# Kernel tuning notes

Hardware: AMD Instinct MI355X
Metric: run time of the kernel (lower is better)

## Reference

```python
import jax, jax.numpy as jnp
import numpy as np

N, E, B, F_IN, C, K = 200000, 3200000, 128, 128, 10, 30
D_CAT = 97  # 32+32+32+1 concatenated GCN outputs


def setup_inputs() -> dict:
    key = jax.random.key(0)
    ks = jax.random.split(key, 12)
    s = 0.1
    return {
        "x": jax.random.normal(ks[0], (N, F_IN), jnp.float32),
        "edge_index": jax.random.randint(ks[1], (2, E), 0, N, jnp.int32),
        "batch": jnp.sort(jax.random.randint(ks[2], (N,), 0, B, jnp.int32)),
        "W1": jax.random.normal(ks[3], (F_IN, 32), jnp.float32) * s,
        "b1": jnp.zeros((32,), jnp.float32),
        "W2": jax.random.normal(ks[4], (32, 32), jnp.float32) * s,
        "b2": jnp.zeros((32,), jnp.float32),
        "W3": jax.random.normal(ks[5], (32, 32), jnp.float32) * s,
        "b3": jnp.zeros((32,), jnp.float32),
        "W4": jax.random.normal(ks[6], (32, 1), jnp.float32) * s,
        "b4": jnp.zeros((1,), jnp.float32),
        "conv5_w": jax.random.normal(ks[7], (16, 1, 97), jnp.float32) * s,
        "conv5_b": jnp.zeros((16,), jnp.float32),
        "conv6_w": jax.random.normal(ks[8], (32, 16, 5), jnp.float32) * s,
        "conv6_b": jnp.zeros((32,), jnp.float32),
        "fc1_w": jax.random.normal(ks[9], (352, 128), jnp.float32) * s,
        "fc1_b": jnp.zeros((128,), jnp.float32),
        "fc2_w": jax.random.normal(ks[10], (128, C), jnp.float32) * s,
        "fc2_b": jnp.zeros((C,), jnp.float32),
    }


def _gcn(x, W, b, src, dst, enorm, self_norm):
    # PyG GCNConv: h = xW; out = sum_j norm_ij * h_j (incl. self loop) + b
    h = x @ W
    agg = jax.ops.segment_sum(h[src] * enorm[:, None], dst, num_segments=h.shape[0])
    return agg + h * self_norm[:, None] + b


def _conv1d(x, w, b, stride):
    y = jax.lax.conv_general_dilated(x, w, (stride,), 'VALID',
                                     dimension_numbers=('NCH', 'OIH', 'NCH'))
    return y + b[None, :, None]


def reference(x, edge_index, batch, W1, b1, W2, b2, W3, b3, W4, b4,
              conv5_w, conv5_b, conv6_w, conv6_b, fc1_w, fc1_b, fc2_w, fc2_b):
    src, dst = edge_index[0], edge_index[1]
    # remove_self_loops (zero edge weight) then GCN adds self loop of weight 1
    w = (src != dst).astype(x.dtype)
    deg = jax.ops.segment_sum(w, dst, num_segments=N) + 1.0
    dinv = jax.lax.rsqrt(deg)
    enorm = w * dinv[src] * dinv[dst]   # per-edge sym norm
    self_norm = 1.0 / deg               # self-loop norm = dinv[i]^2

    x1 = jnp.tanh(_gcn(x, W1, b1, src, dst, enorm, self_norm))
    x2 = jnp.tanh(_gcn(x1, W2, b2, src, dst, enorm, self_norm))
    x3 = jnp.tanh(_gcn(x2, W3, b3, src, dst, enorm, self_norm))
    x4 = jnp.tanh(_gcn(x3, W4, b4, src, dst, enorm, self_norm))
    xc = jnp.concatenate([x1, x2, x3, x4], axis=-1)  # [N, 97]

    # SortAggregation(k=30): per-graph top-k nodes by last channel (descending)
    keyf = xc[:, -1]
    graph_ids = jnp.arange(B, dtype=batch.dtype)
    scores = jnp.where(batch[None, :] == graph_ids[:, None], keyf[None, :],
                       jnp.float32(-jnp.inf))         # [B, N]
    topv, topi = jax.lax.top_k(scores, K)              # [B, K]
    feats = xc[topi]                                   # [B, K, 97]
    feats = jnp.where(jnp.isfinite(topv)[..., None], feats, 0.0)  # pad rows -> 0
    z = feats.reshape(B, 1, K * D_CAT)                 # [B, 1, 2910]

    z = jax.nn.relu(_conv1d(z, conv5_w, conv5_b, 97))  # [B, 16, 30]
    z = jax.lax.reduce_window(z, -jnp.inf, jax.lax.max,
                              (1, 1, 2), (1, 1, 2), 'VALID')  # [B, 16, 15]
    z = jax.nn.relu(_conv1d(z, conv6_w, conv6_b, 1))   # [B, 32, 11]
    z = z.reshape(B, -1)                               # [B, 352]
    h = jax.nn.relu(z @ fc1_w + fc1_b)                 # dropout = identity (eval)
    return jax.nn.log_softmax(h @ fc2_w + fc2_b, axis=-1)
```

## Files before the change

kernel.cpp:

```cpp
#include <hip/hip_runtime.h>
#include <math.h>

#define TPB 256
#define TOPK 30
#define NGRAPH 128
#define TKCAP 4096
#define BSHIFT 11
#define NBMAX 128
#define FSHIFT 8
#define NFMAX 800
#define FCAP 4608


__global__ void bhist(const int* __restrict__ src, const int* __restrict__ dst,
                      int* __restrict__ btot, int E) {
    __shared__ int bcnt[NBMAX];
    int t = threadIdx.x;
    int base = blockIdx.x * 2048;
    int lim = E - base; if (lim > 2048) lim = 2048;
    for (int i = t; i < NBMAX; i += 256) bcnt[i] = 0;
    __syncthreads();
    for (int i = t; i < lim; i += 256) {
        int s = src[base + i], d = dst[base + i];
        if (s != d) atomicAdd(&bcnt[d >> BSHIFT], 1);
    }
    __syncthreads();
    for (int i = t; i < NBMAX; i += 256)
        if (bcnt[i] > 0) atomicAdd(&btot[i], bcnt[i]);
}

__global__ void bucket_scan(const int* __restrict__ btot, int* __restrict__ bbase,
                            int nbuckets) {
    __shared__ int ls[NBMAX];
    int t = threadIdx.x;
    int v = (t < nbuckets) ? btot[t] : 0;
    ls[t] = v;
    __syncthreads();
    for (int o = 1; o < NBMAX; o <<= 1) {
        int x = 0;
        if (t >= o) x = ls[t - o];
        __syncthreads();
        ls[t] += x;
        __syncthreads();
    }
    if (t < nbuckets) bbase[t] = ls[t] - v;
}

__global__ void bin_edges(const int* __restrict__ src, const int* __restrict__ dst,
                          const int* __restrict__ bbase_g, int* __restrict__ gcur,
                          int2* __restrict__ scratch, int E) {
    __shared__ int2 eds[2048];
    __shared__ int bcnt[NBMAX], bbase[NBMAX], boff[NBMAX];
    int t = threadIdx.x;
    int base = blockIdx.x * 2048;
    int lim = E - base; if (lim > 2048) lim = 2048;
    for (int i = t; i < NBMAX; i += 256) { bcnt[i] = 0; boff[i] = 0; }
    __syncthreads();
    for (int i = t; i < lim; i += 256) {
        int s = src[base + i], d = dst[base + i];
        if (s == d) d = -1;
        eds[i] = make_int2(s, d);
        if (d >= 0) atomicAdd(&bcnt[d >> BSHIFT], 1);
    }
    __syncthreads();
    for (int i = t; i < NBMAX; i += 256) {
        if (bcnt[i] > 0)
            bbase[i] = bbase_g[i] + atomicAdd(&gcur[i], bcnt[i]);
    }
    __syncthreads();
    for (int i = t; i < lim; i += 256) {
        int2 ed = eds[i];
        if (ed.y >= 0) {
            int b = ed.y >> BSHIFT;
            int pos = bbase[b] + atomicAdd(&boff[b], 1);
            scratch[pos] = ed;
        }
    }
}

__global__ void bucket_count(const int2* __restrict__ scratch,
                             const int* __restrict__ bbase, const int* __restrict__ btot,
                             int* __restrict__ rowptr, float* __restrict__ dinv,
                             float* __restrict__ snorm, int N, int NB) {
    __shared__ int hist[1 << BSHIFT];
    __shared__ int ls2[256];
    int b = blockIdx.x, t = threadIdx.x;
    int nlo = b << BSHIFT;
    int nn = N - nlo; if (nn > (1 << BSHIFT)) nn = 1 << BSHIFT;
    for (int i = t; i < (1 << BSHIFT); i += 256) hist[i] = 0;
    __syncthreads();
    int lo = bbase[b], hi = lo + btot[b];
    for (int e = lo + t; e < hi; e += 256)
        atomicAdd(&hist[scratch[e].y - nlo], 1);
    __syncthreads();
    int loc[8]; int run = 0;
    #pragma unroll
    for (int j = 0; j < 8; ++j) { loc[j] = run; run += hist[t * 8 + j]; }
    ls2[t] = run;
    __syncthreads();
    for (int o = 1; o < 256; o <<= 1) {
        int x = (t >= o) ? ls2[t - o] : 0;
        __syncthreads();
        ls2[t] += x;
        __syncthreads();
    }
    int base = bbase[b] + ls2[t] - run;
    #pragma unroll
    for (int j = 0; j < 8; ++j) {
        int i = t * 8 + j;
        if (i < nn) {
            rowptr[nlo + i] = base + loc[j];
            int c = hist[i];
            float deg = (float)c + 1.0f;
            dinv[nlo + i] = 1.0f / sqrtf(deg);
            snorm[nlo + i] = 1.0f / deg;
        }
    }
    if (b == NB - 1 && t == 0) rowptr[N] = bbase[b] + btot[b];
}

__global__ void bin2(const int2* __restrict__ scratch, const int* __restrict__ rowptr,
                     int* __restrict__ fcur, int2* __restrict__ scratch2, int N, int E) {
    __shared__ int fcnt[NFMAX], fbase[NFMAX], foff[NFMAX];
    int t = threadIdx.x;
    int En = rowptr[N];
    int base = blockIdx.x * 8192;
    if (base >= En) return;
    int lim = En - base; if (lim > 8192) lim = 8192;
    for (int i = t; i < NFMAX; i += 256) { fcnt[i] = 0; foff[i] = 0; }
    __syncthreads();
    for (int i = t; i < lim; i += 256) {
        int d = scratch[base + i].y;
        atomicAdd(&fcnt[d >> FSHIFT], 1);
    }
    __syncthreads();
    for (int fi = t; fi < NFMAX; fi += 256) {
        if (fcnt[fi] > 0)
            fbase[fi] = rowptr[fi << FSHIFT] + atomicAdd(&fcur[fi], fcnt[fi]);
    }
    __syncthreads();
    for (int i = t; i < lim; i += 256) {
        int2 ed = scratch[base + i];
        int fi = ed.y >> FSHIFT;
        int pos = fbase[fi] + atomicAdd(&foff[fi], 1);
        scratch2[pos] = ed;
    }
}

__global__ __launch_bounds__(256) void scatter_sort(const int2* __restrict__ scratch2,
                                                    const int* __restrict__ rowptr,
                                                    const float* __restrict__ dinv,
                                                    int2* __restrict__ eprec, int N) {
    __shared__ int srcA[FCAP], dstA[FCAP], inv[FCAP];
    __shared__ int hist[1 << FSHIFT];
    __shared__ int hcur[1 << FSHIFT];
    int f = blockIdx.x, t = threadIdx.x;
    int nlo = f << FSHIFT;
    int nhi = nlo + (1 << FSHIFT); if (nhi > N) nhi = N;
    int lo = rowptr[nlo], hi = rowptr[nhi];
    int span = hi - lo;
    for (int i = t; i < (1 << FSHIFT); i += 256) hist[i] = 0;
    __syncthreads();
    if (span <= FCAP) {
        for (int i = t; i < span; i += 256) {
            int2 ed = scratch2[lo + i];
            srcA[i] = ed.x; dstA[i] = ed.y;
            atomicAdd(&hist[ed.y - nlo], 1);
        }
        __syncthreads();
        int v = hist[t];
        hcur[t] = v;
        __syncthreads();
        for (int o = 1; o < 256; o <<= 1) {
            int x = (t >= o) ? hcur[t - o] : 0;
            __syncthreads();
            hcur[t] += x;
            __syncthreads();
        }
        int excl = hcur[t] - v;
        __syncthreads();
        hcur[t] = excl;
        __syncthreads();
        for (int i = t; i < span; i += 256) {
            int slot = atomicAdd(&hcur[dstA[i] - nlo], 1);
            inv[slot] = i;
        }
        __syncthreads();
        for (int p = t; p < span; p += 256) {
            int i = inv[p];
            int s = srcA[i], d = dstA[i];
            eprec[lo + p] = make_int2(s, __float_as_int(dinv[s] * dinv[d]));
        }
    } else {
        for (int e = lo + t; e < hi; e += 256) {
            int2 ed = scratch2[e];
            int d = ed.y;
            int p = rowptr[d] + atomicAdd(&hist[d - nlo], 1);
            eprec[p] = make_int2(ed.x, __float_as_int(dinv[ed.x] * dinv[d]));
        }
    }
}


__global__ void mm_128_32(const float* __restrict__ X, const float* __restrict__ W,
                          float* __restrict__ H, int n) {
    __shared__ float Ws[128 * 32];
    __shared__ float xs[32 * 128];
    int t = threadIdx.x;
    int rbase = blockIdx.x * 32;
    #pragma unroll
    for (int j = 0; j < 4; ++j) {
        int idx = t + 256 * j;
        *(float4*)(Ws + idx * 4) = *(const float4*)(W + idx * 4);
        int row = rbase + (idx >> 5);
        float4 v = make_float4(0.f, 0.f, 0.f, 0.f);
        if (row < n) v = *(const float4*)(X + (long)rbase * 128 + idx * 4);
        *(float4*)(xs + idx * 4) = v;
    }
    __syncthreads();
    int c4 = (t & 7) * 4, r = t >> 3;
    int row = rbase + r;
    if (row >= n) return;
    float ac0 = 0.f, ac1 = 0.f, ac2 = 0.f, ac3 = 0.f;
    #pragma unroll 8
    for (int k0 = 0; k0 < 128; k0 += 4) {
        float4 xv = *(const float4*)(xs + r * 128 + k0);
        #pragma unroll
        for (int j = 0; j < 4; ++j) {
            float xj = (j == 0) ? xv.x : (j == 1) ? xv.y : (j == 2) ? xv.z : xv.w;
            float4 wv = *(const float4*)(Ws + (k0 + j) * 32 + c4);
            ac0 += xj * wv.x; ac1 += xj * wv.y; ac2 += xj * wv.z; ac3 += xj * wv.w;
        }
    }
    *(float4*)(H + (long)row * 32 + c4) = make_float4(ac0, ac1, ac2, ac3);
}

__global__ void mm_32_32(const float* __restrict__ X, const float* __restrict__ W,
                         float* __restrict__ H, int n) {
    __shared__ float Ws[32 * 32];
    __shared__ float xs[32 * 32];
    int t = threadIdx.x;
    int rbase = blockIdx.x * 32;
    {
        *(float4*)(Ws + t * 4) = *(const float4*)(W + t * 4);
        int row = rbase + (t >> 3);
        float4 v = make_float4(0.f, 0.f, 0.f, 0.f);
        if (row < n) v = *(const float4*)(X + (long)rbase * 32 + t * 4);
        *(float4*)(xs + t * 4) = v;
    }
    __syncthreads();
    int c4 = (t & 7) * 4, r = t >> 3;
    int row = rbase + r;
    if (row >= n) return;
    float ac0 = 0.f, ac1 = 0.f, ac2 = 0.f, ac3 = 0.f;
    #pragma unroll
    for (int k0 = 0; k0 < 32; k0 += 4) {
        float4 xv = *(const float4*)(xs + r * 32 + k0);
        #pragma unroll
        for (int j = 0; j < 4; ++j) {
            float xj = (j == 0) ? xv.x : (j == 1) ? xv.y : (j == 2) ? xv.z : xv.w;
            float4 wv = *(const float4*)(Ws + (k0 + j) * 32 + c4);
            ac0 += xj * wv.x; ac1 += xj * wv.y; ac2 += xj * wv.z; ac3 += xj * wv.w;
        }
    }
    *(float4*)(H + (long)row * 32 + c4) = make_float4(ac0, ac1, ac2, ac3);
}

__global__ void mm_32_1(const float* __restrict__ X, const float* __restrict__ W,
                        float* __restrict__ H4, int n) {
    int gid = blockIdx.x * blockDim.x + threadIdx.x;
    int node = gid >> 3, l = gid & 7;
    if (node >= n) return;
    float4 v = *(const float4*)(X + (long)node * 32 + l * 4);
    float s = v.x * W[l * 4] + v.y * W[l * 4 + 1] + v.z * W[l * 4 + 2] + v.w * W[l * 4 + 3];
    s += __shfl_xor(s, 1, 64);
    s += __shfl_xor(s, 2, 64);
    s += __shfl_xor(s, 4, 64);
    if (l == 0) H4[node] = s;
}


__global__ void agg32(const float* __restrict__ H, const int2* __restrict__ eprec,
                      const int* __restrict__ rowptr,
                      const float* __restrict__ snorm, const float* __restrict__ bias,
                      float* __restrict__ OUT, int n) {
    int gid = blockIdx.x * blockDim.x + threadIdx.x;
    int node = gid >> 3, l = gid & 7;
    if (node >= n) return;
    int beg = rowptr[node], end = rowptr[node + 1];
    float ax = 0.f, ay = 0.f, az = 0.f, aw = 0.f;
    int e0 = beg;
    for (; e0 + 8 <= end; e0 += 8) {
        int2 ed = eprec[e0 + l];
        int ss[8]; float ww[8];
        #pragma unroll
        for (int j = 0; j < 8; ++j) {
            ss[j] = __shfl(ed.x, j, 8);
            ww[j] = __shfl(__int_as_float(ed.y), j, 8);
        }
        float4 hv[8];
        #pragma unroll
        for (int j = 0; j < 8; ++j)
            hv[j] = *(const float4*)(H + (long)ss[j] * 32 + l * 4);
        #pragma unroll
        for (int j = 0; j < 8; ++j) {
            ax += hv[j].x * ww[j]; ay += hv[j].y * ww[j];
            az += hv[j].z * ww[j]; aw += hv[j].w * ww[j];
        }
    }
    if (e0 < end) {
        int m = end - e0;
        int2 ed = (l < m) ? eprec[e0 + l] : make_int2(0, 0);
        for (int j = 0; j < m; ++j) {
            int s = __shfl(ed.x, j, 8);
            float w = __shfl(__int_as_float(ed.y), j, 8);
            float4 hv = *(const float4*)(H + (long)s * 32 + l * 4);
            ax += hv.x * w; ay += hv.y * w; az += hv.z * w; aw += hv.w * w;
        }
    }
    float sn = snorm[node];
    float4 hv = *(const float4*)(H + (long)node * 32 + l * 4);
    float4 bv = *(const float4*)(bias + l * 4);
    float4 o;
    o.x = tanhf(ax + hv.x * sn + bv.x);
    o.y = tanhf(ay + hv.y * sn + bv.y);
    o.z = tanhf(az + hv.z * sn + bv.z);
    o.w = tanhf(aw + hv.w * sn + bv.w);
    *(float4*)(OUT + (long)node * 32 + l * 4) = o;
}

__global__ void agg1(const float* __restrict__ H4, const int2* __restrict__ eprec,
                     const int* __restrict__ rowptr,
                     const float* __restrict__ snorm, const float* __restrict__ b4,
                     float* __restrict__ X4, int n) {
    int node = blockIdx.x * blockDim.x + threadIdx.x;
    if (node >= n) return;
    int beg = rowptr[node], end = rowptr[node + 1];
    float acc = 0.f;
    for (int e = beg; e < end; ++e) {
        int2 ed = eprec[e];
        acc += H4[ed.x] * __int_as_float(ed.y);
    }
    X4[node] = tanhf(acc + H4[node] * snorm[node] + b4[0]);
}


__global__ __launch_bounds__(256) void topk_head(
        const float* __restrict__ x1, const float* __restrict__ x2,
        const float* __restrict__ x3, const float* __restrict__ x4,
        const int* __restrict__ batch, int Nn,
        const float* __restrict__ w5, const float* __restrict__ b5,
        const float* __restrict__ w6, const float* __restrict__ b6,
        const float* __restrict__ fw1, const float* __restrict__ fb1,
        const float* __restrict__ fw2, const float* __restrict__ fb2,
        float* __restrict__ out) {
    int g = blockIdx.x;
    int t = threadIdx.x;
    __shared__ int topi_l[TOPK];
    __shared__ int selg[TOPK];
    __shared__ int begend[2];
    __shared__ float vals[TKCAP];
    __shared__ float wbv[4];
    __shared__ int wbi[4];
    __shared__ float feats[TOPK][97];
    __shared__ float c5[16][30];
    __shared__ float p6[16][15];
    __shared__ float z[352];
    __shared__ float hh[128];
    __shared__ float oo[10];

    if (t == 0) {
        int lo = 0, hi = Nn;
        while (lo < hi) { int m = (lo + hi) >> 1; if (batch[m] < g) lo = m + 1; else hi = m; }
        begend[0] = lo;
        lo = 0; hi = Nn;
        while (lo < hi) { int m = (lo + hi) >> 1; if (batch[m] < g + 1) lo = m + 1; else hi = m; }
        begend[1] = lo;
    }
    __syncthreads();
    int beg = begend[0], end = begend[1];
    int range = end - beg;

    if (range <= 2048) {
        if (t < 64) {
            float rv[32];
            #pragma unroll
            for (int j = 0; j < 32; ++j) {
                int i = t + (j << 6);
                rv[j] = (i < range) ? x4[beg + i] : -INFINITY;
            }
            for (int k = 0; k < TOPK; ++k) {
                float best = -INFINITY;
                int bj = -1;
                #pragma unroll
                for (int j = 0; j < 32; ++j)
                    if (rv[j] > best) { best = rv[j]; bj = j; }
                int bi = (bj < 0) ? 0x7fffffff : (bj << 6) + t;
                #pragma unroll
                for (int off = 1; off < 64; off <<= 1) {
                    float ov = __shfl_xor(best, off, 64);
                    int oi = __shfl_xor(bi, off, 64);
                    if (ov > best || (ov == best && oi < bi)) { best = ov; bi = oi; }
                }
                if (t == 0)
                    topi_l[k] = (bi == 0x7fffffff) ? -1 : beg + bi;
                if (bi != 0x7fffffff && (bi & 63) == t) {
                    int wj = bi >> 6;
                    #pragma unroll
                    for (int j = 0; j < 32; ++j)
                        if (j == wj) rv[j] = -INFINITY;
                }
            }
        }
    } else {
        int lim = range < TKCAP ? range : TKCAP;
        for (int i = t; i < lim; i += 256) vals[i] = x4[beg + i];
        __syncthreads();
        for (int k = 0; k < TOPK; ++k) {
            float best = -INFINITY;
            int bi = 0x7fffffff;
            for (int i = t; i < lim; i += 256) {
                float v = vals[i];
                if (v > best) { best = v; bi = i; }
            }
            for (int i = TKCAP + t; i < range; i += 256) {
                int gi = beg + i;
                bool taken = false;
                for (int j = 0; j < k; ++j)
                    if (selg[j] == gi) { taken = true; break; }
                if (taken) continue;
                float v = x4[gi];
                if (v > best || (v == best && i < bi)) { best = v; bi = i; }
            }
            #pragma unroll
            for (int off = 1; off < 64; off <<= 1) {
                float ov = __shfl_xor(best, off, 64);
                int oi = __shfl_xor(bi, off, 64);
                if (ov > best || (ov == best && oi < bi)) { best = ov; bi = oi; }
            }
            if ((t & 63) == 0) { wbv[t >> 6] = best; wbi[t >> 6] = bi; }
            __syncthreads();
            if (t == 0) {
                float bv = wbv[0]; int bi0 = wbi[0];
                for (int wv = 1; wv < 4; ++wv)
                    if (wbv[wv] > bv || (wbv[wv] == bv && wbi[wv] < bi0)) { bv = wbv[wv]; bi0 = wbi[wv]; }
                int gl = (bi0 == 0x7fffffff) ? -1 : beg + bi0;
                selg[k] = gl;
                topi_l[k] = gl;
                if (bi0 != 0x7fffffff && bi0 < TKCAP) vals[bi0] = -INFINITY;
            }
            __syncthreads();
        }
    }
    __syncthreads();

    for (int idx = t; idx < TOPK * 97; idx += 256) {
        int k = idx / 97, j = idx % 97;
        int node = topi_l[k];
        float v = 0.f;
        if (node >= 0) {
            if (j < 32) v = x1[(long)node * 32 + j];
            else if (j < 64) v = x2[(long)node * 32 + (j - 32)];
            else if (j < 96) v = x3[(long)node * 32 + (j - 64)];
            else v = x4[node];
        }
        feats[k][j] = v;
    }
    __syncthreads();

    for (int idx = t; idx < 16 * 30; idx += 256) {
        int oc = idx / 30, k = idx % 30;
        float acc = b5[oc];
        for (int j = 0; j < 97; ++j) acc += w5[oc * 97 + j] * feats[k][j];
        c5[oc][k] = fmaxf(acc, 0.f);
    }
    __syncthreads();

    for (int idx = t; idx < 16 * 15; idx += 256) {
        int oc = idx / 15, k = idx % 15;
        p6[oc][k] = fmaxf(c5[oc][2 * k], c5[oc][2 * k + 1]);
    }
    __syncthreads();

    for (int idx = t; idx < 32 * 11; idx += 256) {
        int oc = idx / 11, tt = idx % 11;
        float acc = b6[oc];
        for (int ic = 0; ic < 16; ++ic)
            for (int j = 0; j < 5; ++j)
                acc += w6[(oc * 16 + ic) * 5 + j] * p6[ic][tt + j];
        z[idx] = fmaxf(acc, 0.f);
    }
    __syncthreads();

    if (t < 128) {
        float acc = fb1[t];
        for (int i = 0; i < 352; ++i) acc += z[i] * fw1[i * 128 + t];
        hh[t] = fmaxf(acc, 0.f);
    }
    __syncthreads();

    if (t < 10) {
        float acc = fb2[t];
        for (int j = 0; j < 128; ++j) acc += hh[j] * fw2[j * 10 + t];
        oo[t] = acc;
    }
    __syncthreads();

    if (t < 10) {
        float m = -INFINITY;
        for (int c = 0; c < 10; ++c) m = fmaxf(m, oo[c]);
        float s = 0.f;
        for (int c = 0; c < 10; ++c) s += expf(oo[c] - m);
        out[g * 10 + t] = oo[t] - m - logf(s);
    }
}


extern "C" void kernel_launch(void* const* d_in, const int* in_sizes, int n_in,
                              void* d_out, int out_size, void* d_ws, size_t ws_size,
                              hipStream_t stream) {
    const float* x     = (const float*)d_in[0];
    const int*   ei    = (const int*)d_in[1];
    const int*   batch = (const int*)d_in[2];
    const float* W1 = (const float*)d_in[3];
    const float* b1 = (const float*)d_in[4];
    const float* W2 = (const float*)d_in[5];
    const float* b2 = (const float*)d_in[6];
    const float* W3 = (const float*)d_in[7];
    const float* b3 = (const float*)d_in[8];
    const float* W4 = (const float*)d_in[9];
    const float* b4 = (const float*)d_in[10];
    const float* w5 = (const float*)d_in[11];
    const float* b5 = (const float*)d_in[12];
    const float* w6 = (const float*)d_in[13];
    const float* b6 = (const float*)d_in[14];
    const float* fw1 = (const float*)d_in[15];
    const float* fb1 = (const float*)d_in[16];
    const float* fw2 = (const float*)d_in[17];
    const float* fb2 = (const float*)d_in[18];

    const int N = in_sizes[0] / 128;
    const int E = in_sizes[1] / 2;
    const int* src = ei;
    const int* dst = ei + E;

    char* w = (char*)d_ws;
    size_t off = 0;
    auto alloc = [&](size_t bytes) -> void* {
        void* p = w + off;
        off = (off + bytes + 255) & ~(size_t)255;
        return p;
    };

    int*   gcur   = (int*)alloc(NBMAX * 4);
    int*   btot   = (int*)alloc(NBMAX * 4);
    int*   fcur   = (int*)alloc(NFMAX * 4);
    int*   bbase  = (int*)alloc(NBMAX * 4);
    int*   rowptr = (int*)alloc((size_t)(N + 1) * 4);
    float* dinv   = (float*)alloc((size_t)N * 4);
    float* snorm  = (float*)alloc((size_t)N * 4);
    int2*  eprec  = (int2*)alloc((size_t)E * 8);
    float* hbuf   = (float*)alloc((size_t)N * 32 * 4);
    float* x1     = (float*)alloc((size_t)N * 32 * 4);
    float* x2     = (float*)alloc((size_t)N * 32 * 4);
    float* x3     = (float*)alloc((size_t)N * 32 * 4);
    float* h4     = (float*)alloc((size_t)N * 4);
    float* x4     = (float*)alloc((size_t)N * 4);

    int2* scratch  = (int2*)hbuf;
    int2* scratch2 = (int2*)x1;

    hipMemsetAsync(gcur, 0, (size_t)(2 * NBMAX + NFMAX) * 4, stream);

    const int NB = (N + (1 << BSHIFT) - 1) >> BSHIFT;
    const int NF = (N + (1 << FSHIFT) - 1) >> FSHIFT;
    const int EB = (E + 2047) / 2048;

    bhist<<<EB, TPB, 0, stream>>>(src, dst, btot, E);
    bucket_scan<<<1, NBMAX, 0, stream>>>(btot, bbase, NB);
    bin_edges<<<EB, TPB, 0, stream>>>(src, dst, bbase, gcur, scratch, E);
    bucket_count<<<NB, TPB, 0, stream>>>(scratch, bbase, btot, rowptr, dinv, snorm, N, NB);
    bin2<<<(E + 8191) / 8192, TPB, 0, stream>>>(scratch, rowptr, fcur, scratch2, N, E);
    scatter_sort<<<NF, 256, 0, stream>>>(scratch2, rowptr, dinv, eprec, N);

    mm_128_32<<<(N + 31) / 32, 256, 0, stream>>>(x, W1, hbuf, N);
    agg32<<<((size_t)N * 8 + TPB - 1) / TPB, TPB, 0, stream>>>(hbuf, eprec, rowptr,
                                                               snorm, b1, x1, N);
    mm_32_32<<<(N + 31) / 32, 256, 0, stream>>>(x1, W2, hbuf, N);
    agg32<<<((size_t)N * 8 + TPB - 1) / TPB, TPB, 0, stream>>>(hbuf, eprec, rowptr,
                                                               snorm, b2, x2, N);
    mm_32_32<<<(N + 31) / 32, 256, 0, stream>>>(x2, W3, hbuf, N);
    agg32<<<((size_t)N * 8 + TPB - 1) / TPB, TPB, 0, stream>>>(hbuf, eprec, rowptr,
                                                               snorm, b3, x3, N);
    mm_32_1<<<((size_t)N * 8 + TPB - 1) / TPB, TPB, 0, stream>>>(x3, W4, h4, N);
    agg1<<<(N + TPB - 1) / TPB, TPB, 0, stream>>>(h4, eprec, rowptr, snorm, b4, x4, N);

    topk_head<<<NGRAPH, 256, 0, stream>>>(x1, x2, x3, x4, batch, N,
                                          w5, b5, w6, b6, fw1, fb1, fw2, fb2,
                                          (float*)d_out);
}
```

Baseline: 565.2 us.

## Precompute graph boundaries and split top-k selection across four wavefronts

A new graph_start kernel computes per-graph start offsets from the sorted batch array once, so topk_head no longer runs two serial binary searches in a single thread. The small-graph top-k path now has each of the four wavefronts select a local top-30 over a quarter of the nodes. One wavefront then merges the 120 candidates, which replaces 32-register-per-lane selection on a single wave. This adds an extra small kernel launch and a shared-memory merge stage.

```diff
diff --git a/kernel.cpp b/kernel.cpp
--- a/kernel.cpp
+++ b/kernel.cpp
@@ -345,10 +345,23 @@
 }
 
 
+__global__ void graph_start(const int* __restrict__ batch, int* __restrict__ gstart,
+                            int n, int B) {
+    int i = blockIdx.x * blockDim.x + threadIdx.x;
+    if (i >= n) return;
+    int b = batch[i];
+    int bp = (i == 0) ? -1 : batch[i - 1];
+    for (int g = bp + 1; g <= b; ++g) gstart[g] = i;
+    if (i == n - 1) {
+        for (int g = b + 1; g <= B; ++g) gstart[g] = n;
+    }
+}
+
+
 __global__ __launch_bounds__(256) void topk_head(
         const float* __restrict__ x1, const float* __restrict__ x2,
         const float* __restrict__ x3, const float* __restrict__ x4,
-        const int* __restrict__ batch, int Nn,
+        const int* __restrict__ gstart,
         const float* __restrict__ w5, const float* __restrict__ b5,
         const float* __restrict__ w6, const float* __restrict__ b6,
         const float* __restrict__ fw1, const float* __restrict__ fb1,
@@ -358,7 +371,8 @@
     int t = threadIdx.x;
     __shared__ int topi_l[TOPK];
     __shared__ int selg[TOPK];
-    __shared__ int begend[2];
+    __shared__ float lv[4 * TOPK];
+    __shared__ int li[4 * TOPK];
     __shared__ float vals[TKCAP];
     __shared__ float wbv[4];
     __shared__ int wbi[4];
@@ -369,33 +383,51 @@
     __shared__ float hh[128];
     __shared__ float oo[10];
 
-    if (t == 0) {
-        int lo = 0, hi = Nn;
-        while (lo < hi) { int m = (lo + hi) >> 1; if (batch[m] < g) lo = m + 1; else hi = m; }
-        begend[0] = lo;
-        lo = 0; hi = Nn;
-        while (lo < hi) { int m = (lo + hi) >> 1; if (batch[m] < g + 1) lo = m + 1; else hi = m; }
-        begend[1] = lo;
-    }
-    __syncthreads();
-    int beg = begend[0], end = begend[1];
+    int beg = gstart[g], end = gstart[g + 1];
     int range = end - beg;
 
     if (range <= 2048) {
+        int wv = t >> 6, l = t & 63;
+        int chunk = (range + 3) >> 2;
+        int cbeg = wv * chunk;
+        int cend = cbeg + chunk; if (cend > range) cend = range;
+        float rv[8];
+        #pragma unroll
+        for (int j = 0; j < 8; ++j) {
+            int i = cbeg + l + (j << 6);
+            rv[j] = (i < cend) ? x4[beg + i] : -INFINITY;
+        }
+        for (int k = 0; k < TOPK; ++k) {
+            float best = -INFINITY;
+            int bj = -1;
+            #pragma unroll
+            for (int j = 0; j < 8; ++j)
+                if (rv[j] > best) { best = rv[j]; bj = j; }
+            int bi = (bj < 0) ? 0x7fffffff : cbeg + (bj << 6) + l;
+            #pragma unroll
+            for (int off = 1; off < 64; off <<= 1) {
+                float ov = __shfl_xor(best, off, 64);
+                int oi = __shfl_xor(bi, off, 64);
+                if (ov > best || (ov == best && oi < bi)) { best = ov; bi = oi; }
+            }
+            if (l == 0) { lv[wv * TOPK + k] = best; li[wv * TOPK + k] = bi; }
+            if (bi != 0x7fffffff && ((bi - cbeg) & 63) == l) {
+                int wj = (bi - cbeg) >> 6;
+                #pragma unroll
+                for (int j = 0; j < 8; ++j)
+                    if (j == wj) rv[j] = -INFINITY;
+            }
+        }
+        __syncthreads();
         if (t < 64) {
-            float rv[32];
-            #pragma unroll
-            for (int j = 0; j < 32; ++j) {
-                int i = t + (j << 6);
-                rv[j] = (i < range) ? x4[beg + i] : -INFINITY;
-            }
+            float mv0 = lv[t];
+            int   mi0 = li[t];
+            int i1 = t + 64;
+            float mv1 = (i1 < 120) ? lv[i1] : -INFINITY;
+            int   mi1 = (i1 < 120) ? li[i1] : 0x7fffffff;
             for (int k = 0; k < TOPK; ++k) {
-                float best = -INFINITY;
-                int bj = -1;
-                #pragma unroll
-                for (int j = 0; j < 32; ++j)
-                    if (rv[j] > best) { best = rv[j]; bj = j; }
-                int bi = (bj < 0) ? 0x7fffffff : (bj << 6) + t;
+                float best = mv0; int bi = mi0;
+                if (mv1 > best || (mv1 == best && mi1 < bi)) { best = mv1; bi = mi1; }
                 #pragma unroll
                 for (int off = 1; off < 64; off <<= 1) {
                     float ov = __shfl_xor(best, off, 64);
@@ -404,12 +436,8 @@
                 }
                 if (t == 0)
                     topi_l[k] = (bi == 0x7fffffff) ? -1 : beg + bi;
-                if (bi != 0x7fffffff && (bi & 63) == t) {
-                    int wj = bi >> 6;
-                    #pragma unroll
-                    for (int j = 0; j < 32; ++j)
-                        if (j == wj) rv[j] = -INFINITY;
-                }
+                if (mi0 == bi) mv0 = -INFINITY;
+                if (mi1 == bi) mv1 = -INFINITY;
             }
         }
     } else {
@@ -442,8 +470,8 @@
             __syncthreads();
             if (t == 0) {
                 float bv = wbv[0]; int bi0 = wbi[0];
-                for (int wv = 1; wv < 4; ++wv)
-                    if (wbv[wv] > bv || (wbv[wv] == bv && wbi[wv] < bi0)) { bv = wbv[wv]; bi0 = wbi[wv]; }
+                for (int wq = 1; wq < 4; ++wq)
+                    if (wbv[wq] > bv || (wbv[wq] == bv && wbi[wq] < bi0)) { bv = wbv[wq]; bi0 = wbi[wq]; }
                 int gl = (bi0 == 0x7fffffff) ? -1 : beg + bi0;
                 selg[k] = gl;
                 topi_l[k] = gl;
@@ -556,6 +584,7 @@
     int*   btot   = (int*)alloc(NBMAX * 4);
     int*   fcur   = (int*)alloc(NFMAX * 4);
     int*   bbase  = (int*)alloc(NBMAX * 4);
+    int*   gstart = (int*)alloc((size_t)(NGRAPH + 1) * 4);
     int*   rowptr = (int*)alloc((size_t)(N + 1) * 4);
     float* dinv   = (float*)alloc((size_t)N * 4);
     float* snorm  = (float*)alloc((size_t)N * 4);
@@ -576,6 +605,7 @@
     const int NF = (N + (1 << FSHIFT) - 1) >> FSHIFT;
     const int EB = (E + 2047) / 2048;
 
+    graph_start<<<(N + TPB - 1) / TPB, TPB, 0, stream>>>(batch, gstart, N, NGRAPH);
     bhist<<<EB, TPB, 0, stream>>>(src, dst, btot, E);
     bucket_scan<<<1, NBMAX, 0, stream>>>(btot, bbase, NB);
     bin_edges<<<EB, TPB, 0, stream>>>(src, dst, bbase, gcur, scratch, E);
@@ -595,7 +625,7 @@
     mm_32_1<<<((size_t)N * 8 + TPB - 1) / TPB, TPB, 0, stream>>>(x3, W4, h4, N);
     agg1<<<(N + TPB - 1) / TPB, TPB, 0, stream>>>(h4, eprec, rowptr, snorm, b4, x4, N);
 
-    topk_head<<<NGRAPH, 256, 0, stream>>>(x1, x2, x3, x4, batch, N,
+    topk_head<<<NGRAPH, 256, 0, stream>>>(x1, x2, x3, x4, gstart,
                                           w5, b5, w6, b6, fw1, fb1, fw2, fb2,
                                           (float*)d_out);
 }
```

New measurement: 568.8 us. No clear change (+0.6%).
